# Kernel tuning notes

Hardware: AMD Instinct MI355X
Metric: run time of the kernel (lower is better)

The kernel has to match this reference:

```python
import jax, jax.numpy as jnp
import numpy as np

B=4; TEXT_LEN=64; IMG=256; P=16; DIM=1024; HEADS=16; LAYERS=2; MLP=4; VOCAB=50000; TDIM=256; MAXTXT=2048
HP=IMG//P; NPATCH=HP*HP; HD=DIM//HEADS; EPS=1e-5

def _ln(x, g, b):
    m = jnp.mean(x, -1, keepdims=True)
    v = jnp.mean((x - m) ** 2, -1, keepdims=True)
    return (x - m) / jnp.sqrt(v + EPS) * g + b

def _rope_cos_sin(n, d):
    inv = 1.0 / (10000.0 ** (jnp.arange(0, d, 2, dtype=jnp.float32) / d))
    f = jnp.outer(jnp.arange(n, dtype=jnp.float32), inv)
    e = jnp.concatenate([f, f], -1)  # [n, d]
    return jnp.cos(e), jnp.sin(e)

def _rot_half(x):
    # matches torch: cat((-x[...,1::2], x[...,::2]), -1)
    return jnp.concatenate([-x[..., 1::2], x[..., ::2]], -1)

def _forward(noisy_images, text_tokens, timesteps, W_tok, pos_text, W_patch, pos_img, cls_tok,
             W_t1, b_t1, W_t2, b_t2, ln1_g, ln1_b, Wq, Wk, Wv, Wo, ln2_g, ln2_b,
             Wm1, Wm2, Wada, b_ada, fn_g, fn_b, W_final, b_final):
    Bn = noisy_images.shape[0]
    # text embed: one_hot @ W_tok.T == gather of columns of W_tok [DIM, VOCAB]
    text_emb = jnp.transpose(jnp.take(W_tok, text_tokens, axis=1), (1, 2, 0)) + pos_text[:, :TEXT_LEN]
    # image patches: [B,3,HP,P,HP,P] -> [B,HP,WP,C,P,P] -> [B,NPATCH, 3*P*P]
    patches = noisy_images.reshape(Bn, 3, HP, P, HP, P).transpose(0, 2, 4, 1, 3, 5).reshape(Bn, NPATCH, 3 * P * P)
    img_emb = patches @ W_patch.T + pos_img
    img_emb = jnp.concatenate([jnp.broadcast_to(cls_tok, (Bn, 1, DIM)), img_emb], 1)
    x = jnp.concatenate([text_emb, img_emb], 1)  # [B, N, DIM]
    N = x.shape[1]
    # sinusoidal timestep embedding (dim=256)
    half = TDIM // 2
    freqs = jnp.exp(-jnp.log(10000.0) * jnp.arange(half, dtype=jnp.float32) / half)
    args = timesteps.astype(jnp.float32)[:, None] * freqs[None]
    temb_raw = jnp.concatenate([jnp.cos(args), jnp.sin(args)], -1)
    t_emb = jax.nn.silu(temb_raw @ W_t1.T + b_t1) @ W_t2.T + b_t2  # [B, DIM]
    cos, sin = _rope_cos_sin(N, HD)
    scale = HD ** -0.5
    for l in range(LAYERS):
        mod = jax.nn.silu(t_emb) @ Wada[l].T + b_ada[l]
        sh_msa, sc_msa, g_msa, sh_mlp, sc_mlp, g_mlp = jnp.split(mod, 6, -1)
        xn = _ln(x, ln1_g[l], ln1_b[l]) * (1 + sc_msa[:, None]) + sh_msa[:, None]
        q = (xn @ Wq[l].T).reshape(Bn, N, HEADS, HD).transpose(0, 2, 1, 3)
        k = (xn @ Wk[l].T).reshape(Bn, N, HEADS, HD).transpose(0, 2, 1, 3)
        v = (xn @ Wv[l].T).reshape(Bn, N, HEADS, HD).transpose(0, 2, 1, 3)
        q = q * cos + _rot_half(q) * sin
        k = k * cos + _rot_half(k) * sin
        att = jax.nn.softmax(jnp.einsum('bhnd,bhmd->bhnm', q, k) * scale, -1)
        o = jnp.einsum('bhnm,bhmd->bhnd', att, v).transpose(0, 2, 1, 3).reshape(Bn, N, DIM)
        x = x + g_msa[:, None] * (o @ Wo[l].T)
        xn2 = _ln(x, ln2_g[l], ln2_b[l]) * (1 + sc_mlp[:, None]) + sh_mlp[:, None]
        mlp = jax.nn.gelu(xn2 @ Wm1[l].T, approximate=False) @ Wm2[l].T
        x = x + g_mlp[:, None] * mlp
    img_tok = x[:, TEXT_LEN + 1:]
    out = _ln(img_tok, fn_g, fn_b) @ W_final.T + b_final  # [B, NPATCH, 3*P*P]
    out = out.reshape(Bn, HP, HP, 3, P, P).transpose(0, 3, 1, 4, 2, 5).reshape(Bn, 3, IMG, IMG)
    return out

def setup_inputs() -> dict:
    key = jax.random.key(0)
    ks = jax.random.split(key, 24)
    def n(k, shape, s=0.02):
        return (jax.random.normal(k, shape, jnp.float32) * s).astype(jnp.float32)
    inp = {}
    inp['noisy_images'] = jax.random.normal(ks[0], (B, 3, IMG, IMG), jnp.float32)
    inp['text_tokens'] = jax.random.randint(ks[1], (B, TEXT_LEN), 0, VOCAB)
    inp['timesteps'] = jax.random.randint(ks[2], (B,), 0, 1000)
    inp['W_tok'] = n(ks[3], (DIM, VOCAB))
    inp['pos_text'] = n(ks[4], (1, MAXTXT, DIM))
    inp['W_patch'] = n(ks[5], (DIM, 3 * P * P))
    inp['pos_img'] = n(ks[6], (1, NPATCH, DIM))
    inp['cls_tok'] = n(ks[7], (1, 1, DIM))
    inp['W_t1'] = n(ks[8], (DIM, TDIM)); inp['b_t1'] = jnp.zeros((DIM,), jnp.float32)
    inp['W_t2'] = n(ks[9], (DIM, DIM)); inp['b_t2'] = jnp.zeros((DIM,), jnp.float32)
    inp['ln1_g'] = jnp.ones((LAYERS, DIM), jnp.float32); inp['ln1_b'] = jnp.zeros((LAYERS, DIM), jnp.float32)
    inp['Wq'] = n(ks[10], (LAYERS, DIM, DIM))
    inp['Wk'] = n(ks[11], (LAYERS, DIM, DIM))
    inp['Wv'] = n(ks[12], (LAYERS, DIM, DIM))
    inp['Wo'] = n(ks[13], (LAYERS, DIM, DIM))
    inp['ln2_g'] = jnp.ones((LAYERS, DIM), jnp.float32); inp['ln2_b'] = jnp.zeros((LAYERS, DIM), jnp.float32)
    inp['Wm1'] = n(ks[14], (LAYERS, MLP * DIM, DIM))
    inp['Wm2'] = n(ks[15], (LAYERS, DIM, MLP * DIM))
    inp['Wada'] = n(ks[16], (LAYERS, 6 * DIM, DIM)); inp['b_ada'] = jnp.zeros((LAYERS, 6 * DIM), jnp.float32)
    inp['fn_g'] = jnp.ones((DIM,), jnp.float32); inp['fn_b'] = jnp.zeros((DIM,), jnp.float32)
    inp['W_final'] = n(ks[17], (3 * P * P, DIM)); inp['b_final'] = jnp.zeros((3 * P * P,), jnp.float32)
    return inp

def reference(noisy_images, text_tokens, timesteps, W_tok, pos_text, W_patch, pos_img, cls_tok,
              W_t1, b_t1, W_t2, b_t2, ln1_g, ln1_b, Wq, Wk, Wv, Wo, ln2_g, ln2_b,
              Wm1, Wm2, Wada, b_ada, fn_g, fn_b, W_final, b_final):
    return _forward(noisy_images, text_tokens, timesteps, W_tok, pos_text, W_patch, pos_img, cls_tok,
                    W_t1, b_t1, W_t2, b_t2, ln1_g, ln1_b, Wq, Wk, Wv, Wo, ln2_g, ln2_b,
                    Wm1, Wm2, Wada, b_ada, fn_g, fn_b, W_final, b_final)
```

## Files before the change

kernel.cpp:

```cpp
#include <hip/hip_runtime.h>
#include <math.h>

constexpr int kBn    = 4;
constexpr int kText  = 64;
constexpr int kImg   = 256;
constexpr int kDim   = 1024;
constexpr int kHeads = 16;
constexpr int kHd    = 64;
constexpr int kNp    = 256;
constexpr int kTok   = 321;
constexpr int kVocab = 50000;
constexpr int kTdim  = 256;
constexpr int kMlp   = 4096;
constexpr int kScLd  = 328;
constexpr float kEps = 1e-5f;

typedef __attribute__((ext_vector_type(8))) short short8;
typedef __attribute__((ext_vector_type(4))) float f32x4;

__device__ __forceinline__ short f2bf(float x) {
  unsigned u = __builtin_bit_cast(unsigned, x);
  unsigned r = (u + 0x7FFFu + ((u >> 16) & 1u)) >> 16;
  return (short)r;
}

struct GemmM {
  const short* A; const short* B; float* C; const float* E;
  int M, N, K, lda, ldb, ldc;
  long sA0, sA1, sB0, sB1, sC0, sC1;
  int innerB, ldE, rowsPB;
  float alpha;
  int nSplit, splitLen;
  long partStride;
};

template<int EPI, bool PART, bool OUTBF>
__global__ __launch_bounds__(256) void gemm_mfma(GemmM p) {
  int bz = blockIdx.z;
  int split = 0;
  if (PART) { split = bz % p.nSplit; bz /= p.nSplit; }
  int b1 = bz % p.innerB, b0 = bz / p.innerB;
  const short* A = p.A + b0*p.sA0 + b1*p.sA1;
  const short* B = p.B + b0*p.sB0 + b1*p.sB1;
  long cbase = b0*p.sC0 + b1*p.sC1 + (PART ? (long)split * p.partStride : 0);
  const float* E = p.E;

  int kBeg = PART ? split * p.splitLen : 0;
  int kEnd = PART ? min(p.K, kBeg + p.splitLen) : p.K;

  __shared__ short As[64*72];
  __shared__ short Bs[64*72];

  int tid  = threadIdx.x;
  int lane = tid & 63, widx = tid >> 6;
  int quad = lane >> 4, ln = lane & 15;
  int wm = (widx >> 1) * 32, wn = (widx & 1) * 32;
  int n0 = blockIdx.x * 64, m0 = blockIdx.y * 64;

  f32x4 zero = {0.f, 0.f, 0.f, 0.f};
  f32x4 acc[2][2];
  acc[0][0] = zero; acc[0][1] = zero; acc[1][0] = zero; acc[1][1] = zero;

  short8 ra[2], rb[2];
  auto issueLoads = [&](int k0) {
#pragma unroll
    for (int r = 0; r < 2; ++r) {
      int c = tid + 256*r;
      int row = c >> 3, kc = c & 7;
      int gk = k0 + kc*8;
      {
        int gm = m0 + row;
        const short* src = A + (long)gm * p.lda + gk;
        if (gm < p.M && gk + 8 <= kEnd) {
          ra[r] = *(const short8*)src;
        } else {
          short8 t = {0,0,0,0,0,0,0,0};
          if (gm < p.M) {
#pragma unroll
            for (int j = 0; j < 8; ++j) if (gk + j < kEnd) t[j] = src[j];
          }
          ra[r] = t;
        }
      }
      {
        int gn = n0 + row;
        const short* src = B + (long)gn * p.ldb + gk;
        if (gn < p.N && gk + 8 <= kEnd) {
          rb[r] = *(const short8*)src;
        } else {
          short8 t = {0,0,0,0,0,0,0,0};
          if (gn < p.N) {
#pragma unroll
            for (int j = 0; j < 8; ++j) if (gk + j < kEnd) t[j] = src[j];
          }
          rb[r] = t;
        }
      }
    }
  };

  issueLoads(kBeg);
  for (int k0 = kBeg; k0 < kEnd; k0 += 64) {
#pragma unroll
    for (int r = 0; r < 2; ++r) {
      int c = tid + 256*r;
      int row = c >> 3, kc = c & 7;
      *(short8*)&As[row*72 + kc*8] = ra[r];
      *(short8*)&Bs[row*72 + kc*8] = rb[r];
    }
    __syncthreads();
    if (k0 + 64 < kEnd) issueLoads(k0 + 64);
#pragma unroll
    for (int ks = 0; ks < 2; ++ks) {
      short8 a0 = *(const short8*)&As[(wm +      ln)*72 + ks*32 + quad*8];
      short8 a1 = *(const short8*)&As[(wm + 16 + ln)*72 + ks*32 + quad*8];
      short8 b0 = *(const short8*)&Bs[(wn +      ln)*72 + ks*32 + quad*8];
      short8 b1 = *(const short8*)&Bs[(wn + 16 + ln)*72 + ks*32 + quad*8];
      acc[0][0] = __builtin_amdgcn_mfma_f32_16x16x32_bf16(a0, b0, acc[0][0], 0, 0, 0);
      acc[0][1] = __builtin_amdgcn_mfma_f32_16x16x32_bf16(a0, b1, acc[0][1], 0, 0, 0);
      acc[1][0] = __builtin_amdgcn_mfma_f32_16x16x32_bf16(a1, b0, acc[1][0], 0, 0, 0);
      acc[1][1] = __builtin_amdgcn_mfma_f32_16x16x32_bf16(a1, b1, acc[1][1], 0, 0, 0);
    }
    __syncthreads();
  }

#pragma unroll
  for (int mi = 0; mi < 2; ++mi)
#pragma unroll
    for (int ni = 0; ni < 2; ++ni)
#pragma unroll
      for (int reg = 0; reg < 4; ++reg) {
        int gm = m0 + wm + mi*16 + quad*4 + reg;
        int gn = n0 + wn + ni*16 + ln;
        if (gm >= p.M || gn >= p.N) continue;
        long co = cbase + (long)gm * p.ldc + gn;
        float v = acc[mi][ni][reg] * p.alpha;
        if (!PART) {
          if (EPI == 1) v += E[gn];
          else if (EPI == 3) v = 0.5f*v*(1.f + erff(v*0.70710678118654752f));
          else if (EPI == 4) v += E[(long)gm*p.ldE + gn];
          else if (EPI == 5) v = p.C[co] + E[(long)(gm / p.rowsPB)*p.ldE + gn] * v;
        }
        if (OUTBF) ((short*)p.C)[co] = f2bf(v);
        else       p.C[co] = v;
      }
}

static GemmM mkm(const short* A, const short* B, float* C,
                 int M, int N, int K, int lda, int ldb, int ldc) {
  GemmM p; p.A = A; p.B = B; p.C = C; p.E = nullptr;
  p.M = M; p.N = N; p.K = K; p.lda = lda; p.ldb = ldb; p.ldc = ldc;
  p.sA0 = p.sA1 = p.sB0 = p.sB1 = p.sC0 = p.sC1 = 0;
  p.innerB = 1; p.ldE = 0; p.rowsPB = 1; p.alpha = 1.f;
  p.nSplit = 1; p.splitLen = 0; p.partStride = 0;
  return p;
}

static void run_gemm(hipStream_t s, int epi, bool outbf, const GemmM& p, int nb) {
  dim3 g((p.N + 63)/64, (p.M + 63)/64, nb), b(256, 1, 1);
  if (outbf) {
    if (epi == 3) gemm_mfma<3,false,true><<<g,b,0,s>>>(p);
    else          gemm_mfma<0,false,true><<<g,b,0,s>>>(p);
    return;
  }
  switch (epi) {
    case 0: gemm_mfma<0,false,false><<<g,b,0,s>>>(p); break;
    case 1: gemm_mfma<1,false,false><<<g,b,0,s>>>(p); break;
    case 4: gemm_mfma<4,false,false><<<g,b,0,s>>>(p); break;
    case 5: gemm_mfma<5,false,false><<<g,b,0,s>>>(p); break;
  }
}

static void run_gemm_part(hipStream_t s, const GemmM& p, int nb) {
  dim3 g((p.N + 63)/64, (p.M + 63)/64, nb * p.nSplit), b(256, 1, 1);
  gemm_mfma<0,true,false><<<g,b,0,s>>>(p);
}

template<int EPI>
__global__ __launch_bounds__(256) void reduce_split(
    const float* __restrict__ part, long partStride, int S,
    float* __restrict__ C, const float* __restrict__ E,
    int Mv, int Nv, int ldc, long sC0, long sC1, int innerB,
    int ldE, int rowsPB, int total) {
  int idx = blockIdx.x*256 + threadIdx.x;
  if (idx >= total) return;
  int n = idx % Nv;
  int m = (idx / Nv) % Mv;
  int bz = idx / (Nv * Mv);
  int b1 = bz % innerB, b0 = bz / innerB;
  long co = b0*sC0 + b1*sC1 + (long)m*ldc + n;
  float v = 0.f;
  for (int s = 0; s < S; ++s) v += part[(long)s*partStride + co];
  if (EPI == 1) v += E[n];
  else if (EPI == 3) v = 0.5f*v*(1.f + erff(v*0.70710678118654752f));
  else if (EPI == 4) v += E[(long)m*ldE + n];
  else if (EPI == 5) v = C[co] + E[(long)(m / rowsPB)*ldE + n] * v;
  C[co] = v;
}

static void run_reduce(hipStream_t st, int epi, const float* part, long pStride, int S,
                       float* C, const float* E, int Mv, int Nv, int ldc,
                       long sC0, long sC1, int innerB, int nbTot, int ldE, int rowsPB) {
  int total = nbTot * Mv * Nv;
  dim3 g((total + 255)/256), b(256);
  switch (epi) {
    case 0: reduce_split<0><<<g,b,0,st>>>(part,pStride,S,C,E,Mv,Nv,ldc,sC0,sC1,innerB,ldE,rowsPB,total); break;
    case 1: reduce_split<1><<<g,b,0,st>>>(part,pStride,S,C,E,Mv,Nv,ldc,sC0,sC1,innerB,ldE,rowsPB,total); break;
    case 3: reduce_split<3><<<g,b,0,st>>>(part,pStride,S,C,E,Mv,Nv,ldc,sC0,sC1,innerB,ldE,rowsPB,total); break;
    case 4: reduce_split<4><<<g,b,0,st>>>(part,pStride,S,C,E,Mv,Nv,ldc,sC0,sC1,innerB,ldE,rowsPB,total); break;
    case 5: reduce_split<5><<<g,b,0,st>>>(part,pStride,S,C,E,Mv,Nv,ldc,sC0,sC1,innerB,ldE,rowsPB,total); break;
  }
}

__global__ __launch_bounds__(256) void cvt_bf16(const float* __restrict__ src,
                                                short* __restrict__ dst, int n8) {
  int i = blockIdx.x*256 + threadIdx.x;
  if (i >= n8) return;
  float4 a = ((const float4*)src)[2*i];
  float4 b = ((const float4*)src)[2*i + 1];
  short8 o;
  o[0]=f2bf(a.x); o[1]=f2bf(a.y); o[2]=f2bf(a.z); o[3]=f2bf(a.w);
  o[4]=f2bf(b.x); o[5]=f2bf(b.y); o[6]=f2bf(b.z); o[7]=f2bf(b.w);
  *(short8*)(dst + 8L*i) = o;
}

static void cvt(hipStream_t s, const float* src, short* dst, long n) {
  long n8 = n / 8;
  cvt_bf16<<<dim3((unsigned)((n8 + 255)/256)), dim3(256), 0, s>>>(src, dst, (int)n8);
}

template<int EPI>
__global__ __launch_bounds__(256) void gemv4(const float* __restrict__ A,
                                             const float* __restrict__ B,
                                             float* __restrict__ C,
                                             const float* __restrict__ bias,
                                             int N, int K, int ldc) {
  int wave = threadIdx.x >> 6, lane = threadIdx.x & 63;
  int n = blockIdx.x * 4 + wave;
  if (n >= N) return;
  const float* Brow = B + (long)n * K;
  float acc0 = 0.f, acc1 = 0.f, acc2 = 0.f, acc3 = 0.f;
  for (int k = lane * 4; k < K; k += 256) {
    float4 b = *(const float4*)(Brow + k);
    float4 a0 = *(const float4*)(A + 0*K + k);
    float4 a1 = *(const float4*)(A + 1*K + k);
    float4 a2 = *(const float4*)(A + 2*K + k);
    float4 a3 = *(const float4*)(A + 3*K + k);
    acc0 += a0.x*b.x + a0.y*b.y + a0.z*b.z + a0.w*b.w;
    acc1 += a1.x*b.x + a1.y*b.y + a1.z*b.z + a1.w*b.w;
    acc2 += a2.x*b.x + a2.y*b.y + a2.z*b.z + a2.w*b.w;
    acc3 += a3.x*b.x + a3.y*b.y + a3.z*b.z + a3.w*b.w;
  }
#pragma unroll
  for (int off = 32; off; off >>= 1) {
    acc0 += __shfl_xor(acc0, off);
    acc1 += __shfl_xor(acc1, off);
    acc2 += __shfl_xor(acc2, off);
    acc3 += __shfl_xor(acc3, off);
  }
  if (lane == 0) {
    float bs = bias[n];
    float v[4] = {acc0 + bs, acc1 + bs, acc2 + bs, acc3 + bs};
#pragma unroll
    for (int m = 0; m < 4; ++m) {
      float x = v[m];
      if (EPI == 2) x = x / (1.f + expf(-x));
      C[(long)m * ldc + n] = x;
    }
  }
}

__global__ void embed_text_cls(const float* __restrict__ Wtok, const int* __restrict__ toks,
                               const float* __restrict__ pos_text, const float* __restrict__ cls_tok,
                               float* __restrict__ x) {
  int idx = blockIdx.x*256 + threadIdx.x;
  int d = idx % kDim;
  int t = (idx / kDim) % (kText + 1);
  int b = idx / (kDim * (kText + 1));
  float v;
  if (t < kText) {
    int tok = toks[b*kText + t];
    v = Wtok[(long)d*kVocab + tok] + pos_text[(long)t*kDim + d];
  } else {
    v = cls_tok[d];
  }
  x[((long)b*kTok + t)*kDim + d] = v;
}

__global__ void extract_patches(const float* __restrict__ img, short* __restrict__ pat) {
  int idx = blockIdx.x*256 + threadIdx.x;
  int k = idx % 768;
  int p = (idx/768) % kNp;
  int b = idx/(768*kNp);
  int c = k >> 8, py = (k >> 4) & 15, px = k & 15;
  int hp = p >> 4, wp = p & 15;
  pat[idx] = f2bf(img[(((long)(b*3 + c))*kImg + hp*16 + py)*kImg + wp*16 + px]);
}

__global__ void time_freqs(const int* __restrict__ ts, float* __restrict__ temb) {
  int b = blockIdx.x, i = threadIdx.x;
  float f = expf(-9.210340371976184f * (float)i / 128.f);
  float a = (float)ts[b] * f;
  temb[b*kTdim + i] = cosf(a);
  temb[b*kTdim + 128 + i] = sinf(a);
}

__global__ void silu_kernel(const float* __restrict__ in, float* __restrict__ outp, int n) {
  int i = blockIdx.x*256 + threadIdx.x;
  if (i < n) { float x = in[i]; outp[i] = x / (1.f + expf(-x)); }
}

__device__ __forceinline__ float block_sum(float v) {
  __shared__ float sh[4];
  for (int off = 32; off; off >>= 1) v += __shfl_down(v, off);
  if ((threadIdx.x & 63) == 0) sh[threadIdx.x >> 6] = v;
  __syncthreads();
  float s = sh[0] + sh[1] + sh[2] + sh[3];
  __syncthreads();
  return s;
}

__global__ __launch_bounds__(256) void ln_mod_kernel(
    const float* __restrict__ x, const float* __restrict__ g, const float* __restrict__ be,
    const float* __restrict__ mod, int shOff, int scOff, short* __restrict__ outp) {
  int row = blockIdx.x;
  int b = row / kTok;
  const float* xr = x + (long)row*kDim;
  float s = 0.f, s2 = 0.f;
  for (int i = threadIdx.x; i < kDim; i += 256) { float v = xr[i]; s += v; s2 += v*v; }
  s = block_sum(s); s2 = block_sum(s2);
  float m = s / kDim;
  float inv = rsqrtf(s2 / kDim - m*m + kEps);
  const float* mb = mod + (long)b*(6*kDim);
  for (int i = threadIdx.x; i < kDim; i += 256) {
    float xn = (xr[i] - m)*inv*g[i] + be[i];
    outp[(long)row*kDim + i] = f2bf(xn*(1.f + mb[scOff + i]) + mb[shOff + i]);
  }
}

__global__ __launch_bounds__(256) void final_ln_kernel(
    const float* __restrict__ x, const float* __restrict__ g, const float* __restrict__ be,
    short* __restrict__ yn) {
  int row = blockIdx.x;
  int b = row / kNp, p = row % kNp;
  const float* xr = x + ((long)(b*kTok + kText + 1 + p))*kDim;
  float s = 0.f, s2 = 0.f;
  for (int i = threadIdx.x; i < kDim; i += 256) { float v = xr[i]; s += v; s2 += v*v; }
  s = block_sum(s); s2 = block_sum(s2);
  float m = s / kDim;
  float inv = rsqrtf(s2 / kDim - m*m + kEps);
  for (int i = threadIdx.x; i < kDim; i += 256)
    yn[(long)row*kDim + i] = f2bf((xr[i] - m)*inv*g[i] + be[i]);
}

__global__ __launch_bounds__(256) void rope_bf16(const float* __restrict__ qkv,
                                                 short* __restrict__ qb,
                                                 short* __restrict__ kb) {
  int idx = blockIdx.x*256 + threadIdx.x;
  int d = idx & (kDim - 1);
  int r = idx >> 10;
  int n = r % kTok;
  int hd = d & 63;
  int j = hd & 31;
  float inv = expf(-9.210340371976184f * (float)j / 32.f);
  float ang = (float)n * inv;
  float c = cosf(ang), s = sinf(ang);
  const float* row = qkv + (long)r * (3*kDim);
  int base = d - hd;
  float qv = row[d], kv = row[kDim + d];
  float qr, kr;
  if (hd < 32) { qr = -row[base + 2*hd + 1];      kr = -row[kDim + base + 2*hd + 1]; }
  else         { qr =  row[base + 2*(hd - 32)];   kr =  row[kDim + base + 2*(hd - 32)]; }
  qb[idx] = f2bf(qv*c + qr*s);
  kb[idx] = f2bf(kv*c + kr*s);
}

__global__ __launch_bounds__(256) void vtrans_kernel(const float* __restrict__ qkv,
                                                     short* __restrict__ vtb) {
  int idx = blockIdx.x*256 + threadIdx.x;
  int tok = idx % kScLd;
  int hd  = (idx / kScLd) % kHd;
  int h   = (idx / (kScLd*kHd)) % kHeads;
  int b   = idx / (kScLd*kHd*kHeads);
  float v = 0.f;
  if (tok < kTok) v = qkv[((long)(b*kTok + tok))*(3*kDim) + 2*kDim + h*kHd + hd];
  vtb[idx] = f2bf(v);
}

__global__ void softmax_rows(float* __restrict__ sc, short* __restrict__ dst,
                             int rowLen, int rowStride) {
  long row = blockIdx.x;
  float* r = sc + row*rowStride;
  short* d = dst + row*rowStride;
  int t = threadIdx.x;
  float mx = -1e30f;
  for (int i = t; i < rowLen; i += 64) mx = fmaxf(mx, r[i]);
  for (int off = 32; off; off >>= 1) mx = fmaxf(mx, __shfl_xor(mx, off));
  float sum = 0.f;
  for (int i = t; i < rowLen; i += 64) { float e = expf(r[i] - mx); r[i] = e; sum += e; }
  for (int off = 32; off; off >>= 1) sum += __shfl_xor(sum, off);
  float invs = 1.f / sum;
  for (int i = t; i < rowLen; i += 64) d[i] = f2bf(r[i] * invs);
}

__global__ void unpatchify(const float* __restrict__ op, float* __restrict__ outp) {
  int idx = blockIdx.x*256 + threadIdx.x;
  int w = idx & 255;
  int h = (idx >> 8) & 255;
  int c = (idx >> 16) % 3;
  int b = idx / (3 * kImg * kImg);
  int hp = h >> 4, py = h & 15, wp = w >> 4, px = w & 15;
  outp[idx] = op[((long)(b*kNp + hp*16 + wp))*768 + c*256 + py*16 + px];
}

extern "C" void kernel_launch(void* const* d_in, const int* in_sizes, int n_in,
                              void* d_out, int out_size, void* d_ws, size_t ws_size,
                              hipStream_t stream) {
  (void)in_sizes; (void)n_in; (void)out_size;
  const float* noisy    = (const float*)d_in[0];
  const int*   toks     = (const int*)d_in[1];
  const int*   tsteps   = (const int*)d_in[2];
  const float* W_tok    = (const float*)d_in[3];
  const float* pos_text = (const float*)d_in[4];
  const float* W_patch  = (const float*)d_in[5];
  const float* pos_img  = (const float*)d_in[6];
  const float* cls_tok  = (const float*)d_in[7];
  const float* W_t1     = (const float*)d_in[8];
  const float* b_t1     = (const float*)d_in[9];
  const float* W_t2     = (const float*)d_in[10];
  const float* b_t2     = (const float*)d_in[11];
  const float* ln1_g    = (const float*)d_in[12];
  const float* ln1_b    = (const float*)d_in[13];
  const float* Wq       = (const float*)d_in[14];
  const float* Wk       = (const float*)d_in[15];
  const float* Wv       = (const float*)d_in[16];
  const float* Wo       = (const float*)d_in[17];
  const float* ln2_g    = (const float*)d_in[18];
  const float* ln2_b    = (const float*)d_in[19];
  const float* Wm1      = (const float*)d_in[20];
  const float* Wm2      = (const float*)d_in[21];
  const float* Wada     = (const float*)d_in[22];
  const float* b_ada    = (const float*)d_in[23];
  const float* fn_g     = (const float*)d_in[24];
  const float* fn_b     = (const float*)d_in[25];
  const float* W_final  = (const float*)d_in[26];
  const float* b_final  = (const float*)d_in[27];
  float* out = (float*)d_out;

  float* ws = (float*)d_ws;
  auto alloc = [&](long nf) { float* r = ws; ws += nf; return r; };

  const long seqSz = (long)kBn * kTok * kDim;
  float* x    = alloc(seqSz);
  float* qkv  = alloc((long)kBn*kTok*3*kDim);
  float* sc   = alloc((long)kBn*kHeads*kTok*kScLd);
  short* xnb  = (short*)alloc(seqSz/2);
  short* qb   = (short*)alloc(seqSz/2);
  short* kb   = (short*)alloc(seqSz/2);
  short* ob   = (short*)alloc(seqSz/2);
  short* vtb  = (short*)alloc((long)kBn*kHeads*kHd*kScLd/2);
  short* scb  = (short*)alloc((long)kBn*kHeads*kTok*kScLd/2);
  short* patb = (short*)alloc((long)kBn*kNp*768/2);
  short* ynb  = (short*)alloc((long)kBn*kNp*kDim/2);
  short* wbuf = (short*)alloc((long)kMlp*kDim/2);
  float* temb = alloc(kBn*kTdim);
  float* t1   = alloc(kBn*kDim);
  float* temb2= alloc(kBn*kDim);
  float* st   = alloc(kBn*kDim);
  float* mod  = alloc(2L*kBn*6*kDim);
  short* hb   = (short*)sc;
  float* outp = qkv;

  const long scrStride = seqSz;
  float* scr = alloc(4*scrStride);
  bool split_ok = ((char*)ws - (char*)d_ws) <= (long)ws_size;

  embed_text_cls<<<(kBn*(kText+1)*kDim)/256, 256, 0, stream>>>(W_tok, toks, pos_text, cls_tok, x);
  extract_patches<<<(kBn*kNp*768)/256, 256, 0, stream>>>(noisy, patb);
  cvt(stream, W_patch, wbuf, (long)kDim*768);
  {
    GemmM p = mkm(patb, wbuf, split_ok ? scr : (x + (kText+1)*kDim),
                  kNp, kDim, 768, 768, 768, kDim);
    p.sA0 = (long)kNp*768; p.sC0 = (long)kTok*kDim;
    if (split_ok) {
      p.nSplit = 3; p.splitLen = 256; p.partStride = scrStride;
      run_gemm_part(stream, p, kBn);
      run_reduce(stream, 4, scr, scrStride, 3, x + (kText+1)*kDim, pos_img,
                 kNp, kDim, kDim, (long)kTok*kDim, 0, 1, kBn, kDim, 1);
    } else {
      p.E = pos_img; p.ldE = kDim;
      run_gemm(stream, 4, false, p, kBn);
    }
  }
  time_freqs<<<kBn, 128, 0, stream>>>(tsteps, temb);
  gemv4<2><<<kDim/4, 256, 0, stream>>>(temb, W_t1, t1, b_t1, kDim, kTdim, kDim);
  gemv4<1><<<kDim/4, 256, 0, stream>>>(t1, W_t2, temb2, b_t2, kDim, kDim, kDim);
  silu_kernel<<<(kBn*kDim + 255)/256, 256, 0, stream>>>(temb2, st, kBn*kDim);

  for (int l = 0; l < 2; ++l) {
    const float* Wq_l  = Wq  + (long)l*kDim*kDim;
    const float* Wk_l  = Wk  + (long)l*kDim*kDim;
    const float* Wv_l  = Wv  + (long)l*kDim*kDim;
    const float* Wo_l  = Wo  + (long)l*kDim*kDim;
    const float* Wm1_l = Wm1 + (long)l*kMlp*kDim;
    const float* Wm2_l = Wm2 + (long)l*kDim*kMlp;
    float* mod_l = mod + (long)l*kBn*6*kDim;

    gemv4<1><<<(6*kDim)/4, 256, 0, stream>>>(st, Wada + (long)l*6*kDim*kDim, mod_l,
                                             b_ada + (long)l*6*kDim, 6*kDim, kDim, 6*kDim);

    ln_mod_kernel<<<kBn*kTok, 256, 0, stream>>>(x, ln1_g + l*kDim, ln1_b + l*kDim,
                                                mod_l, 0, kDim, xnb);
    cvt(stream, Wq_l, wbuf,                   (long)kDim*kDim);
    cvt(stream, Wk_l, wbuf +   (long)kDim*kDim, (long)kDim*kDim);
    cvt(stream, Wv_l, wbuf + 2L*(long)kDim*kDim, (long)kDim*kDim);
    {
      GemmM p = mkm(xnb, wbuf, qkv, kBn*kTok, 3*kDim, kDim, kDim, kDim, 3*kDim);
      run_gemm(stream, 0, false, p, 1);
    }
    rope_bf16<<<(int)(seqSz/256), 256, 0, stream>>>(qkv, qb, kb);
    vtrans_kernel<<<(kBn*kHeads*kHd*kScLd)/256, 256, 0, stream>>>(qkv, vtb);

    {
      GemmM p = mkm(qb, kb, sc, kTok, kTok, kHd, kDim, kDim, kScLd);
      p.sA0 = (long)kTok*kDim; p.sA1 = kHd;
      p.sB0 = (long)kTok*kDim; p.sB1 = kHd;
      p.sC0 = (long)kHeads*kTok*kScLd; p.sC1 = (long)kTok*kScLd;
      p.innerB = kHeads; p.alpha = 0.125f;
      run_gemm(stream, 0, false, p, kBn*kHeads);
    }
    softmax_rows<<<kBn*kHeads*kTok, 64, 0, stream>>>(sc, scb, kTok, kScLd);
    {
      GemmM p = mkm(scb, vtb, (float*)ob, kTok, kHd, kTok, kScLd, kScLd, kDim);
      p.sA0 = (long)kHeads*kTok*kScLd; p.sA1 = (long)kTok*kScLd;
      p.sB0 = (long)kHeads*kHd*kScLd;  p.sB1 = (long)kHd*kScLd;
      p.sC0 = (long)kTok*kDim;         p.sC1 = kHd;
      p.innerB = kHeads;
      run_gemm(stream, 0, true, p, kBn*kHeads);
    }
    cvt(stream, Wo_l, wbuf, (long)kDim*kDim);
    {
      GemmM p = mkm(ob, wbuf, split_ok ? scr : x, kBn*kTok, kDim, kDim, kDim, kDim, kDim);
      if (split_ok) {
        p.nSplit = 4; p.splitLen = 256; p.partStride = scrStride;
        run_gemm_part(stream, p, 1);
        run_reduce(stream, 5, scr, scrStride, 4, x, mod_l + 2*kDim,
                   kBn*kTok, kDim, kDim, 0, 0, 1, 1, 6*kDim, kTok);
      } else {
        p.E = mod_l + 2*kDim; p.ldE = 6*kDim; p.rowsPB = kTok;
        run_gemm(stream, 5, false, p, 1);
      }
    }
    ln_mod_kernel<<<kBn*kTok, 256, 0, stream>>>(x, ln2_g + l*kDim, ln2_b + l*kDim,
                                                mod_l, 3*kDim, 4*kDim, xnb);
    cvt(stream, Wm1_l, wbuf, (long)kMlp*kDim);
    {
      GemmM p = mkm(xnb, wbuf, (float*)hb, kBn*kTok, kMlp, kDim, kDim, kDim, kMlp);
      run_gemm(stream, 3, true, p, 1);
    }
    cvt(stream, Wm2_l, wbuf, (long)kMlp*kDim);
    {
      GemmM p = mkm(hb, wbuf, split_ok ? scr : x, kBn*kTok, kDim, kMlp, kMlp, kMlp, kDim);
      if (split_ok) {
        p.nSplit = 4; p.splitLen = 1024; p.partStride = scrStride;
        run_gemm_part(stream, p, 1);
        run_reduce(stream, 5, scr, scrStride, 4, x, mod_l + 5*kDim,
                   kBn*kTok, kDim, kDim, 0, 0, 1, 1, 6*kDim, kTok);
      } else {
        p.E = mod_l + 5*kDim; p.ldE = 6*kDim; p.rowsPB = kTok;
        run_gemm(stream, 5, false, p, 1);
      }
    }
  }

  final_ln_kernel<<<kBn*kNp, 256, 0, stream>>>(x, fn_g, fn_b, ynb);
  cvt(stream, W_final, wbuf, (long)768*kDim);
  {
    GemmM p = mkm(ynb, wbuf, split_ok ? scr : outp, kBn*kNp, 768, kDim, kDim, kDim, 768);
    if (split_ok) {
      p.nSplit = 4; p.splitLen = 256; p.partStride = (long)kBn*kNp*768;
      run_gemm_part(stream, p, 1);
      run_reduce(stream, 1, scr, (long)kBn*kNp*768, 4, outp, b_final,
                 kBn*kNp, 768, 768, 0, 0, 1, 1, 0, 1);
    } else {
      p.E = b_final;
      run_gemm(stream, 1, false, p, 1);
    }
  }
  unpatchify<<<(kBn*3*kImg*kImg)/256, 256, 0, stream>>>(outp, out);
}
```

Baseline: 823.2 us.

## Add 128x128-tile MFMA GEMM kernel and use it for large projections

Introduces a second GEMM kernel that uses 128x128 output tiles, with each of four waves computing a 64x64 subtile (4x4 MFMA accumulators), and software-prefetches the next K tile into registers. The dense projections (patch embed, QKV, Wo, MLP, final) now use it, while the per-head attention GEMMs stay on the 64x64 kernel. The aim is more data reuse per LDS load and fewer global loads per FLOP. In exchange it uses more registers and fewer blocks, which can leave CUs idle on the smaller 1284-row GEMMs, especially the split-K ones.

```diff
diff --git a/kernel.cpp b/kernel.cpp
--- a/kernel.cpp
+++ b/kernel.cpp
@@ -34,6 +34,15 @@
   long partStride;
 };
 
+__device__ __forceinline__ float epi_apply(int EPI, const GemmM& p, const float* E,
+                                           long co, int gm, int gn, float v) {
+  if (EPI == 1) v += E[gn];
+  else if (EPI == 3) v = 0.5f*v*(1.f + erff(v*0.70710678118654752f));
+  else if (EPI == 4) v += E[(long)gm*p.ldE + gn];
+  else if (EPI == 5) v = p.C[co] + E[(long)(gm / p.rowsPB)*p.ldE + gn] * v;
+  return v;
+}
+
 template<int EPI, bool PART, bool OUTBF>
 __global__ __launch_bounds__(256) void gemm_mfma(GemmM p) {
   int bz = blockIdx.z;
@@ -135,12 +144,120 @@
         if (gm >= p.M || gn >= p.N) continue;
         long co = cbase + (long)gm * p.ldc + gn;
         float v = acc[mi][ni][reg] * p.alpha;
-        if (!PART) {
-          if (EPI == 1) v += E[gn];
-          else if (EPI == 3) v = 0.5f*v*(1.f + erff(v*0.70710678118654752f));
-          else if (EPI == 4) v += E[(long)gm*p.ldE + gn];
-          else if (EPI == 5) v = p.C[co] + E[(long)(gm / p.rowsPB)*p.ldE + gn] * v;
+        if (!PART) v = epi_apply(EPI, p, E, co, gm, gn, v);
+        if (OUTBF) ((short*)p.C)[co] = f2bf(v);
+        else       p.C[co] = v;
+      }
+}
+
+template<int EPI, bool PART, bool OUTBF>
+__global__ __launch_bounds__(256) void gemm_mfma128(GemmM p) {
+  int bz = blockIdx.z;
+  int split = 0;
+  if (PART) { split = bz % p.nSplit; bz /= p.nSplit; }
+  int b1 = bz % p.innerB, b0 = bz / p.innerB;
+  const short* A = p.A + b0*p.sA0 + b1*p.sA1;
+  const short* B = p.B + b0*p.sB0 + b1*p.sB1;
+  long cbase = b0*p.sC0 + b1*p.sC1 + (PART ? (long)split * p.partStride : 0);
+  const float* E = p.E;
+
+  int kBeg = PART ? split * p.splitLen : 0;
+  int kEnd = PART ? min(p.K, kBeg + p.splitLen) : p.K;
+
+  __shared__ short As[128*72];
+  __shared__ short Bs[128*72];
+
+  int tid  = threadIdx.x;
+  int lane = tid & 63, widx = tid >> 6;
+  int quad = lane >> 4, ln = lane & 15;
+  int wm = (widx >> 1) * 64, wn = (widx & 1) * 64;
+  int n0 = blockIdx.x * 128, m0 = blockIdx.y * 128;
+
+  f32x4 zero = {0.f, 0.f, 0.f, 0.f};
+  f32x4 acc[4][4];
+#pragma unroll
+  for (int i = 0; i < 4; ++i)
+#pragma unroll
+    for (int j = 0; j < 4; ++j) acc[i][j] = zero;
+
+  short8 ra[4], rb[4];
+  auto issueLoads = [&](int k0) {
+#pragma unroll
+    for (int r = 0; r < 4; ++r) {
+      int c = tid + 256*r;
+      int row = c >> 3, kc = c & 7;
+      int gk = k0 + kc*8;
+      {
+        int gm = m0 + row;
+        const short* src = A + (long)gm * p.lda + gk;
+        if (gm < p.M && gk + 8 <= kEnd) {
+          ra[r] = *(const short8*)src;
+        } else {
+          short8 t = {0,0,0,0,0,0,0,0};
+          if (gm < p.M) {
+#pragma unroll
+            for (int j = 0; j < 8; ++j) if (gk + j < kEnd) t[j] = src[j];
+          }
+          ra[r] = t;
         }
+      }
+      {
+        int gn = n0 + row;
+        const short* src = B + (long)gn * p.ldb + gk;
+        if (gn < p.N && gk + 8 <= kEnd) {
+          rb[r] = *(const short8*)src;
+        } else {
+          short8 t = {0,0,0,0,0,0,0,0};
+          if (gn < p.N) {
+#pragma unroll
+            for (int j = 0; j < 8; ++j) if (gk + j < kEnd) t[j] = src[j];
+          }
+          rb[r] = t;
+        }
+      }
+    }
+  };
+
+  issueLoads(kBeg);
+  for (int k0 = kBeg; k0 < kEnd; k0 += 64) {
+#pragma unroll
+    for (int r = 0; r < 4; ++r) {
+      int c = tid + 256*r;
+      int row = c >> 3, kc = c & 7;
+      *(short8*)&As[row*72 + kc*8] = ra[r];
+      *(short8*)&Bs[row*72 + kc*8] = rb[r];
+    }
+    __syncthreads();
+    if (k0 + 64 < kEnd) issueLoads(k0 + 64);
+#pragma unroll
+    for (int ks = 0; ks < 2; ++ks) {
+      short8 a[4], b[4];
+#pragma unroll
+      for (int i = 0; i < 4; ++i) {
+        a[i] = *(const short8*)&As[(wm + i*16 + ln)*72 + ks*32 + quad*8];
+        b[i] = *(const short8*)&Bs[(wn + i*16 + ln)*72 + ks*32 + quad*8];
+      }
+#pragma unroll
+      for (int mi = 0; mi < 4; ++mi)
+#pragma unroll
+        for (int ni = 0; ni < 4; ++ni)
+          acc[mi][ni] = __builtin_amdgcn_mfma_f32_16x16x32_bf16(a[mi], b[ni], acc[mi][ni], 0, 0, 0);
+    }
+    __syncthreads();
+  }
+
+#pragma unroll
+  for (int mi = 0; mi < 4; ++mi)
+#pragma unroll
+    for (int ni = 0; ni < 4; ++ni)
+#pragma unroll
+      for (int reg = 0; reg < 4; ++reg) {
+        int gm = m0 + wm + mi*16 + quad*4 + reg;
+        int gn = n0 + wn + ni*16 + ln;
+        if (gm >= p.M || gn >= p.N) continue;
+        long co = cbase + (long)gm * p.ldc + gn;
+        float v = acc[mi][ni][reg] * p.alpha;
+        if (!PART) v = epi_apply(EPI, p, E, co, gm, gn, v);
         if (OUTBF) ((short*)p.C)[co] = f2bf(v);
         else       p.C[co] = v;
       }
@@ -156,24 +273,30 @@
   return p;
 }
 
-static void run_gemm(hipStream_t s, int epi, bool outbf, const GemmM& p, int nb) {
+static void run_gemm64(hipStream_t s, bool outbf, const GemmM& p, int nb) {
   dim3 g((p.N + 63)/64, (p.M + 63)/64, nb), b(256, 1, 1);
+  if (outbf) gemm_mfma<0,false,true><<<g,b,0,s>>>(p);
+  else       gemm_mfma<0,false,false><<<g,b,0,s>>>(p);
+}
+
+static void run_gemm128(hipStream_t s, int epi, bool outbf, const GemmM& p, int nb) {
+  dim3 g((p.N + 127)/128, (p.M + 127)/128, nb), b(256, 1, 1);
   if (outbf) {
-    if (epi == 3) gemm_mfma<3,false,true><<<g,b,0,s>>>(p);
-    else          gemm_mfma<0,false,true><<<g,b,0,s>>>(p);
+    if (epi == 3) gemm_mfma128<3,false,true><<<g,b,0,s>>>(p);
+    else          gemm_mfma128<0,false,true><<<g,b,0,s>>>(p);
     return;
   }
   switch (epi) {
-    case 0: gemm_mfma<0,false,false><<<g,b,0,s>>>(p); break;
-    case 1: gemm_mfma<1,false,false><<<g,b,0,s>>>(p); break;
-    case 4: gemm_mfma<4,false,false><<<g,b,0,s>>>(p); break;
-    case 5: gemm_mfma<5,false,false><<<g,b,0,s>>>(p); break;
-  }
-}
-
-static void run_gemm_part(hipStream_t s, const GemmM& p, int nb) {
-  dim3 g((p.N + 63)/64, (p.M + 63)/64, nb * p.nSplit), b(256, 1, 1);
-  gemm_mfma<0,true,false><<<g,b,0,s>>>(p);
+    case 0: gemm_mfma128<0,false,false><<<g,b,0,s>>>(p); break;
+    case 1: gemm_mfma128<1,false,false><<<g,b,0,s>>>(p); break;
+    case 4: gemm_mfma128<4,false,false><<<g,b,0,s>>>(p); break;
+    case 5: gemm_mfma128<5,false,false><<<g,b,0,s>>>(p); break;
+  }
+}
+
+static void run_gemm128_part(hipStream_t s, const GemmM& p, int nb) {
+  dim3 g((p.N + 127)/128, (p.M + 127)/128, nb * p.nSplit), b(256, 1, 1);
+  gemm_mfma128<0,true,false><<<g,b,0,s>>>(p);
 }
 
 template<int EPI>
@@ -206,7 +329,6 @@
   switch (epi) {
     case 0: reduce_split<0><<<g,b,0,st>>>(part,pStride,S,C,E,Mv,Nv,ldc,sC0,sC1,innerB,ldE,rowsPB,total); break;
     case 1: reduce_split<1><<<g,b,0,st>>>(part,pStride,S,C,E,Mv,Nv,ldc,sC0,sC1,innerB,ldE,rowsPB,total); break;
-    case 3: reduce_split<3><<<g,b,0,st>>>(part,pStride,S,C,E,Mv,Nv,ldc,sC0,sC1,innerB,ldE,rowsPB,total); break;
     case 4: reduce_split<4><<<g,b,0,st>>>(part,pStride,S,C,E,Mv,Nv,ldc,sC0,sC1,innerB,ldE,rowsPB,total); break;
     case 5: reduce_split<5><<<g,b,0,st>>>(part,pStride,S,C,E,Mv,Nv,ldc,sC0,sC1,innerB,ldE,rowsPB,total); break;
   }
@@ -484,12 +606,12 @@
     p.sA0 = (long)kNp*768; p.sC0 = (long)kTok*kDim;
     if (split_ok) {
       p.nSplit = 3; p.splitLen = 256; p.partStride = scrStride;
-      run_gemm_part(stream, p, kBn);
+      run_gemm128_part(stream, p, kBn);
       run_reduce(stream, 4, scr, scrStride, 3, x + (kText+1)*kDim, pos_img,
                  kNp, kDim, kDim, (long)kTok*kDim, 0, 1, kBn, kDim, 1);
     } else {
       p.E = pos_img; p.ldE = kDim;
-      run_gemm(stream, 4, false, p, kBn);
+      run_gemm128(stream, 4, false, p, kBn);
     }
   }
   time_freqs<<<kBn, 128, 0, stream>>>(tsteps, temb);
@@ -511,12 +633,12 @@
 
     ln_mod_kernel<<<kBn*kTok, 256, 0, stream>>>(x, ln1_g + l*kDim, ln1_b + l*kDim,
                                                 mod_l, 0, kDim, xnb);
-    cvt(stream, Wq_l, wbuf,                   (long)kDim*kDim);
+    cvt(stream, Wq_l, wbuf,                     (long)kDim*kDim);
     cvt(stream, Wk_l, wbuf +   (long)kDim*kDim, (long)kDim*kDim);
     cvt(stream, Wv_l, wbuf + 2L*(long)kDim*kDim, (long)kDim*kDim);
     {
       GemmM p = mkm(xnb, wbuf, qkv, kBn*kTok, 3*kDim, kDim, kDim, kDim, 3*kDim);
-      run_gemm(stream, 0, false, p, 1);
+      run_gemm128(stream, 0, false, p, 1);
     }
     rope_bf16<<<(int)(seqSz/256), 256, 0, stream>>>(qkv, qb, kb);
     vtrans_kernel<<<(kBn*kHeads*kHd*kScLd)/256, 256, 0, stream>>>(qkv, vtb);
@@ -527,7 +649,7 @@
       p.sB0 = (long)kTok*kDim; p.sB1 = kHd;
       p.sC0 = (long)kHeads*kTok*kScLd; p.sC1 = (long)kTok*kScLd;
       p.innerB = kHeads; p.alpha = 0.125f;
-      run_gemm(stream, 0, false, p, kBn*kHeads);
+      run_gemm64(stream, false, p, kBn*kHeads);
     }
     softmax_rows<<<kBn*kHeads*kTok, 64, 0, stream>>>(sc, scb, kTok, kScLd);
     {
@@ -536,19 +658,19 @@
       p.sB0 = (long)kHeads*kHd*kScLd;  p.sB1 = (long)kHd*kScLd;
       p.sC0 = (long)kTok*kDim;         p.sC1 = kHd;
       p.innerB = kHeads;
-      run_gemm(stream, 0, true, p, kBn*kHeads);
+      run_gemm64(stream, true, p, kBn*kHeads);
     }
     cvt(stream, Wo_l, wbuf, (long)kDim*kDim);
     {
       GemmM p = mkm(ob, wbuf, split_ok ? scr : x, kBn*kTok, kDim, kDim, kDim, kDim, kDim);
       if (split_ok) {
         p.nSplit = 4; p.splitLen = 256; p.partStride = scrStride;
-        run_gemm_part(stream, p, 1);
+        run_gemm128_part(stream, p, 1);
         run_reduce(stream, 5, scr, scrStride, 4, x, mod_l + 2*kDim,
                    kBn*kTok, kDim, kDim, 0, 0, 1, 1, 6*kDim, kTok);
       } else {
         p.E = mod_l + 2*kDim; p.ldE = 6*kDim; p.rowsPB = kTok;
-        run_gemm(stream, 5, false, p, 1);
+        run_gemm128(stream, 5, false, p, 1);
       }
     }
     ln_mod_kernel<<<kBn*kTok, 256, 0, stream>>>(x, ln2_g + l*kDim, ln2_b + l*kDim,
@@ -556,19 +678,19 @@
     cvt(stream, Wm1_l, wbuf, (long)kMlp*kDim);
     {
       GemmM p = mkm(xnb, wbuf, (float*)hb, kBn*kTok, kMlp, kDim, kDim, kDim, kMlp);
-      run_gemm(stream, 3, true, p, 1);
+      run_gemm128(stream, 3, true, p, 1);
     }
     cvt(stream, Wm2_l, wbuf, (long)kMlp*kDim);
     {
       GemmM p = mkm(hb, wbuf, split_ok ? scr : x, kBn*kTok, kDim, kMlp, kMlp, kMlp, kDim);
       if (split_ok) {
         p.nSplit = 4; p.splitLen = 1024; p.partStride = scrStride;
-        run_gemm_part(stream, p, 1);
+        run_gemm128_part(stream, p, 1);
         run_reduce(stream, 5, scr, scrStride, 4, x, mod_l + 5*kDim,
                    kBn*kTok, kDim, kDim, 0, 0, 1, 1, 6*kDim, kTok);
       } else {
         p.E = mod_l + 5*kDim; p.ldE = 6*kDim; p.rowsPB = kTok;
-        run_gemm(stream, 5, false, p, 1);
+        run_gemm128(stream, 5, false, p, 1);
       }
     }
   }
@@ -579,12 +701,12 @@
     GemmM p = mkm(ynb, wbuf, split_ok ? scr : outp, kBn*kNp, 768, kDim, kDim, kDim, 768);
     if (split_ok) {
       p.nSplit = 4; p.splitLen = 256; p.partStride = (long)kBn*kNp*768;
-      run_gemm_part(stream, p, 1);
+      run_gemm128_part(stream, p, 1);
       run_reduce(stream, 1, scr, (long)kBn*kNp*768, 4, outp, b_final,
                  kBn*kNp, 768, 768, 0, 0, 1, 1, 0, 1);
     } else {
       p.E = b_final;
-      run_gemm(stream, 1, false, p, 1);
+      run_gemm128(stream, 1, false, p, 1);
     }
   }
   unpatchify<<<(kBn*3*kImg*kImg)/256, 256, 0, stream>>>(outp, out);
```

Result: slower. 873.4 us (+6.1%).
